# Kernel tuning notes

Hardware: AMD Instinct MI355X
Metric: run time of the kernel (lower is better)

The kernel has to match this reference:

```python
import jax, jax.numpy as jnp
import numpy as np
from jax import lax

N, D, H, E = 8192, 1024, 4096, 8


def setup_inputs() -> dict:
    key = jax.random.key(0)
    ks = jax.random.split(key, 4)
    return {
        "x": jax.random.normal(ks[0], (N, D), dtype=jnp.float32),
        "wg": jax.random.normal(ks[1], (D, E), dtype=jnp.float32) * 0.001,
        "fc1_w": jax.random.normal(ks[2], (E, D, H), dtype=jnp.float32) * 0.001,
        "fc1_b": jnp.zeros((E, 1, H), dtype=jnp.float32),
        "fc2_w": jax.random.normal(ks[3], (E, H, D), dtype=jnp.float32) * 0.001,
        "fc2_b": jnp.zeros((E, 1, D), dtype=jnp.float32),
        "k": 2,
    }


def reference(x, wg, fc1_w, fc1_b, fc2_w, fc2_b, k):
    n, d = x.shape
    e = wg.shape[1]
    cap = (k * n) // e  # expert capacity (capacity factor 1.0)

    # --- gate ---
    scores = jax.nn.softmax(x @ wg, axis=-1)          # [N,E]
    topv, topi = lax.top_k(scores, k)                 # [N,k]

    # --- top-k routing: position of each (token, slot) within its expert buffer ---
    masks = jax.nn.one_hot(topi, e, dtype=jnp.int32)  # [N,k,E]
    # slot-major priority: all slot-0 assignments before slot-1
    m = jnp.transpose(masks, (1, 0, 2)).reshape(k * n, e)
    pos_flat = jnp.cumsum(m, axis=0) - m              # position before own assignment
    pos = jnp.sum(pos_flat * m, axis=1).reshape(k, n).T   # [N,k]
    valid = pos < cap                                  # capacity overflow -> dropped

    # --- load-balance aux loss (top-1 fraction * mean gate prob) ---
    me = scores.mean(axis=0)                           # [E]
    ce = masks[:, 0, :].astype(scores.dtype).mean(axis=0)
    l_aux = e * jnp.sum(me * ce)

    # --- encode (dispatch): scatter tokens into [E, C, D] buffers ---
    w = valid.astype(x.dtype)                          # [N,k]
    flat_idx = topi * cap + jnp.where(valid, pos, 0)   # [N,k]
    contrib = (x[:, None, :] * w[:, :, None]).reshape(-1, d)
    dispatched = jnp.zeros((e * cap, d), x.dtype).at[flat_idx.reshape(-1)].add(contrib)
    dispatched = dispatched.reshape(e, cap, d)

    # --- batched expert FFN (all-to-all is identity on one device) ---
    h = jax.nn.relu(jnp.einsum('ecd,edh->ech', dispatched, fc1_w) + fc1_b)
    y = jnp.einsum('ech,ehd->ecd', h, fc2_w) + fc2_b   # [E,C,D]

    # --- decode (combine): gather back and weight by gate scores ---
    gathered = y.reshape(e * cap, d)[flat_idx]         # [N,k,D]
    output = jnp.einsum('nk,nkd->nd', topv * w, gathered)
    return output, l_aux
```

## Files before the change

kernel.cpp:

```cpp
#include <hip/hip_runtime.h>
#include <hip/hip_bf16.h>
#include <stdint.h>

#define N_TOK 8192
#define DMODEL 1024
#define HDIM 4096
#define NEXP 8
#define CAP 2048
#define GATE_BLOCKS (N_TOK / 4)

typedef float floatx4 __attribute__((ext_vector_type(4)));
typedef int int32x4_t __attribute__((ext_vector_type(4)));
typedef int int32x8_t __attribute__((ext_vector_type(8)));

static __device__ __forceinline__ void async_copy16(const void* g, void* l) {
  __builtin_amdgcn_global_load_lds(
      (const __attribute__((address_space(1))) void*)g,
      (__attribute__((address_space(3))) void*)l, 16, 0, 0);
}

static __device__ __forceinline__ unsigned int pk4_fp8(float a, float b, float c, float d) {
  int r = __builtin_amdgcn_cvt_pk_fp8_f32(a, b, 0, 0);
  r = __builtin_amdgcn_cvt_pk_fp8_f32(c, d, r, 1);
  return (unsigned int)r;
}

static __device__ __forceinline__ unsigned short f2bf(float f) {
  union { float f; uint32_t u; } v; v.f = f;
  uint32_t r = (v.u + 0x7FFFu + ((v.u >> 16) & 1u)) >> 16;
  return (unsigned short)r;
}

static __device__ __forceinline__ float bf2f(unsigned short u) {
  union { float f; uint32_t u32; } v; v.u32 = ((uint32_t)u) << 16;
  return v.f;
}

__global__ __launch_bounds__(256) void gate_kernel(
    const float* __restrict__ x, const float* __restrict__ wg,
    float* __restrict__ topv, int* __restrict__ topi,
    float* __restrict__ me_part, int* __restrict__ ce_part) {
  __shared__ float sm_p[4][NEXP];
  __shared__ int sm_i0[4];
  int wave = threadIdx.x >> 6;
  int lane = threadIdx.x & 63;
  int n = blockIdx.x * 4 + wave;
  float acc[NEXP];
#pragma unroll
  for (int e = 0; e < NEXP; e++) acc[e] = 0.f;
  const float* xr = x + (size_t)n * DMODEL;
#pragma unroll 4
  for (int i = 0; i < DMODEL / 64; i++) {
    int idx = lane + 64 * i;
    float xv = xr[idx];
    const float4* wr = (const float4*)(wg + (size_t)idx * NEXP);
    float4 w0 = wr[0], w1 = wr[1];
    acc[0] += xv * w0.x; acc[1] += xv * w0.y;
    acc[2] += xv * w0.z; acc[3] += xv * w0.w;
    acc[4] += xv * w1.x; acc[5] += xv * w1.y;
    acc[6] += xv * w1.z; acc[7] += xv * w1.w;
  }
#pragma unroll
  for (int e = 0; e < NEXP; e++) {
    float v = acc[e];
#pragma unroll
    for (int off = 32; off > 0; off >>= 1) v += __shfl_down(v, off, 64);
    acc[e] = v;
  }
  if (lane == 0) {
    float mx = acc[0];
#pragma unroll
    for (int e = 1; e < NEXP; e++) mx = fmaxf(mx, acc[e]);
    float p[NEXP]; float s = 0.f;
#pragma unroll
    for (int e = 0; e < NEXP; e++) { p[e] = expf(acc[e] - mx); s += p[e]; }
    float inv = 1.f / s;
#pragma unroll
    for (int e = 0; e < NEXP; e++) p[e] *= inv;
    int i0 = 0; float v0 = p[0];
#pragma unroll
    for (int e = 1; e < NEXP; e++) if (p[e] > v0) { v0 = p[e]; i0 = e; }
    int i1 = -1; float v1 = -1.f;
#pragma unroll
    for (int e = 0; e < NEXP; e++) {
      if (e == i0) continue;
      if (p[e] > v1) { v1 = p[e]; i1 = e; }
    }
    topv[n * 2] = v0; topv[n * 2 + 1] = v1;
    topi[n * 2] = i0; topi[n * 2 + 1] = i1;
#pragma unroll
    for (int e = 0; e < NEXP; e++) sm_p[wave][e] = p[e];
    sm_i0[wave] = i0;
  }
  __syncthreads();
  if (threadIdx.x < NEXP) {
    int e = threadIdx.x;
    float pm = 0.f; int cc = 0;
#pragma unroll
    for (int w = 0; w < 4; w++) {
      pm += sm_p[w][e];
      cc += (sm_i0[w] == e) ? 1 : 0;
    }
    me_part[blockIdx.x * NEXP + e] = pm;
    ce_part[blockIdx.x * NEXP + e] = cc;
  }
}

__global__ __launch_bounds__(1024) void scan_kernel(
    const int* __restrict__ topi, const float* __restrict__ topv,
    int* __restrict__ flat_idx, float* __restrict__ cw,
    const float* __restrict__ me_part, const int* __restrict__ ce_part,
    float* __restrict__ out_laux) {
  __shared__ int hist[16][NEXP];
  __shared__ int base[NEXP];
  __shared__ float redm[NEXP][2];
  __shared__ float redc[NEXP][2];
  int tid = threadIdx.x;
  int w = tid >> 6, lane = tid & 63;
  if (tid < NEXP) base[tid] = 0;
  int vals[16];
#pragma unroll
  for (int c = 0; c < 16; c++) {
    int j = c * 1024 + tid;
    vals[c] = topi[(size_t)(j & 8191) * 2 + (j >> 13)];
  }
  __syncthreads();
  for (int c = 0; c < 16; c++) {
    int j = c * 1024 + tid;
    int slot = j >> 13;
    int n = j & 8191;
    int e = vals[c];
    int rank = 0;
#pragma unroll
    for (int ee = 0; ee < NEXP; ee++) {
      unsigned long long m = __ballot(e == ee);
      if (e == ee) rank = __popcll(m & ((1ull << lane) - 1ull));
      if (lane == ee) hist[w][ee] = __popcll(m);
    }
    __syncthreads();
    if (tid < NEXP) {
      int run = base[tid];
#pragma unroll
      for (int ww = 0; ww < 16; ww++) {
        int t = hist[ww][tid];
        hist[ww][tid] = run;
        run += t;
      }
      base[tid] = run;
    }
    __syncthreads();
    int pos = hist[w][e] + rank;
    bool valid = pos < CAP;
    flat_idx[n * 2 + slot] = e * CAP + (valid ? pos : 0);
    cw[n * 2 + slot] = valid ? topv[n * 2 + slot] : 0.f;
    __syncthreads();
  }
  {
    int e2 = tid >> 7, c2 = tid & 127;
    float pm = 0.f, cc = 0.f;
    for (int b = c2; b < GATE_BLOCKS; b += 128) {
      pm += me_part[b * NEXP + e2];
      cc += (float)ce_part[b * NEXP + e2];
    }
#pragma unroll
    for (int off = 32; off > 0; off >>= 1) {
      pm += __shfl_down(pm, off, 64);
      cc += __shfl_down(cc, off, 64);
    }
    if ((tid & 63) == 0) {
      redm[e2][(tid >> 6) & 1] = pm;
      redc[e2][(tid >> 6) & 1] = cc;
    }
    __syncthreads();
    if (tid == 0) {
      float s = 0.f;
#pragma unroll
      for (int ee = 0; ee < NEXP; ee++) {
        float tm2 = redm[ee][0] + redm[ee][1];
        float tc2 = redc[ee][0] + redc[ee][1];
        s += (tm2 / (float)N_TOK) * (tc2 / (float)N_TOK);
      }
      *out_laux = (float)NEXP * s;
    }
  }
}

__global__ __launch_bounds__(256) void transpose_cvt_fp8_both(
    const float* __restrict__ in1, unsigned char* __restrict__ out1,
    const float* __restrict__ in2, unsigned char* __restrict__ out2) {
  __shared__ float tile[32][129];
  int z = blockIdx.z;
  const float* in; unsigned char* out; int R, C, bx, by, zz;
  if (z < 8) {
    in = in1; out = out1; R = DMODEL; C = HDIM; zz = z;
    bx = blockIdx.x; by = blockIdx.y;
  } else {
    in = in2; out = out2; R = HDIM; C = DMODEL; zz = z - 8;
    bx = blockIdx.x & 31; by = blockIdx.y * 4 + (blockIdx.x >> 5);
  }
  const float* inp = in + (size_t)zz * R * C;
  unsigned char* outp = out + (size_t)zz * R * C;
  int c0 = bx * 32, r0 = by * 128;
  int t = threadIdx.x;
#pragma unroll
  for (int p = 0; p < 4; p++) {
    int r = p * 32 + (t >> 3);
    int c4 = (t & 7) * 4;
    float4 v = *(const float4*)(inp + (size_t)(r0 + r) * C + c0 + c4);
    tile[c4 + 0][r] = v.x; tile[c4 + 1][r] = v.y;
    tile[c4 + 2][r] = v.z; tile[c4 + 3][r] = v.w;
  }
  __syncthreads();
  int c = t >> 3, r16 = (t & 7) * 16;
  unsigned int w[4];
#pragma unroll
  for (int j = 0; j < 4; j++) {
    float a = tile[c][r16 + j * 4 + 0] * 512.f;
    float b = tile[c][r16 + j * 4 + 1] * 512.f;
    float cc2 = tile[c][r16 + j * 4 + 2] * 512.f;
    float d = tile[c][r16 + j * 4 + 3] * 512.f;
    w[j] = pk4_fp8(a, b, cc2, d);
  }
  uint4 o; o.x = w[0]; o.y = w[1]; o.z = w[2]; o.w = w[3];
  *(uint4*)(outp + (size_t)(c0 + c) * R + r0 + r16) = o;
}

__global__ __launch_bounds__(64) void dispatch_kernel(
    const float* __restrict__ x, const int* __restrict__ flat_idx,
    const float* __restrict__ cw, unsigned char* __restrict__ disp) {
  int a = blockIdx.x;
  if (cw[a] == 0.f) return;
  int n = a >> 1;
  int f = flat_idx[a];
  int lane = threadIdx.x;
  const float4* xr = (const float4*)(x + (size_t)n * DMODEL);
  unsigned int* dr = (unsigned int*)(disp + (size_t)f * DMODEL);
#pragma unroll
  for (int i = 0; i < 4; i++) {
    float4 v = xr[lane + 64 * i];
    dr[lane + 64 * i] = pk4_fp8(v.x, v.y, v.z, v.w);
  }
}

template <int K_DIM, bool RELU, int OUT_MODE>
__global__ __launch_bounds__(256) void gemm_fp8_kernel(
    const unsigned char* __restrict__ A, const unsigned char* __restrict__ BT,
    const float* __restrict__ bias, void* __restrict__ Cout, int M, int Ncols,
    float inv_scale, float out_mult) {
  constexpr int BK = 128;
  constexpr int NSTAGE = K_DIM / BK;
  static_assert(NSTAGE >= 2, "need >=2 K stages for the 2-deep pipeline");
  __shared__ unsigned char As[2][128 * BK];
  __shared__ unsigned char Bs[2][128 * BK];

  int e = blockIdx.z, tm = blockIdx.y, tn = blockIdx.x;
  const unsigned char* Ae = A + (size_t)e * M * K_DIM + (size_t)tm * 128 * K_DIM;
  const unsigned char* Be = BT + (size_t)e * Ncols * K_DIM + (size_t)tn * 128 * K_DIM;
  int wv = threadIdx.x >> 6, l = threadIdx.x & 63;
  int wm = wv >> 1, wn = wv & 1;
  int l15 = l & 15, quad = l >> 4;
  int rbase = wv * 8 + (l >> 3);
  int cg = (l & 7) ^ ((l >> 3) & 7);
  floatx4 acc[4][4] = {};

#define STAGE_LOADS(k0, buf)                                                   \
  {                                                                            \
    _Pragma("unroll") for (int i = 0; i < 4; i++) {                            \
      int r = rbase + i * 32;                                                  \
      async_copy16(Ae + (size_t)r * K_DIM + (k0) + cg * 16,                    \
                   &As[buf][i * 4096 + wv * 1024]);                            \
      async_copy16(Be + (size_t)r * K_DIM + (k0) + cg * 16,                    \
                   &Bs[buf][i * 4096 + wv * 1024]);                            \
    }                                                                          \
  }

#define READ_AF(mi)                                                            \
  {                                                                            \
    int m = wm * 64 + (mi) * 16 + l15;                                         \
    int x0 = (quad * 2) ^ (m & 7), x1 = (quad * 2 + 1) ^ (m & 7);              \
    int32x4_t lo = *(const int32x4_t*)(&As[cur][m * 128 + x0 * 16]);           \
    int32x4_t hi = *(const int32x4_t*)(&As[cur][m * 128 + x1 * 16]);           \
    af[mi] = __builtin_shufflevector(lo, hi, 0, 1, 2, 3, 4, 5, 6, 7);          \
  }

  STAGE_LOADS(0, 0);
  STAGE_LOADS(BK, 1);
#pragma unroll
  for (int s = 0; s < NSTAGE; s++) {
    const int cur = s & 1;
    if (s + 1 < NSTAGE)
      asm volatile("s_waitcnt vmcnt(8)" ::: "memory");
    else
      asm volatile("s_waitcnt vmcnt(0)" ::: "memory");
    __builtin_amdgcn_s_barrier();
    int32x8_t af[4], bf[4];
#pragma unroll
    for (int ni = 0; ni < 4; ni++) {
      int m = wn * 64 + ni * 16 + l15;
      int x0 = (quad * 2) ^ (m & 7), x1 = (quad * 2 + 1) ^ (m & 7);
      int32x4_t lo = *(const int32x4_t*)(&Bs[cur][m * 128 + x0 * 16]);
      int32x4_t hi = *(const int32x4_t*)(&Bs[cur][m * 128 + x1 * 16]);
      bf[ni] = __builtin_shufflevector(lo, hi, 0, 1, 2, 3, 4, 5, 6, 7);
    }
    READ_AF(0);
    __builtin_amdgcn_sched_barrier(0);
    READ_AF(1);
    READ_AF(2);
    READ_AF(3);
    __builtin_amdgcn_sched_barrier(0);
    __builtin_amdgcn_s_setprio(1);
    asm volatile("s_waitcnt lgkmcnt(6)" ::: "memory");
    __builtin_amdgcn_sched_barrier(0);
#pragma unroll
    for (int ni = 0; ni < 4; ni++)
      acc[0][ni] = __builtin_amdgcn_mfma_scale_f32_16x16x128_f8f6f4(
          af[0], bf[ni], acc[0][ni], 0, 0, 0, 0x7F7F7F7F, 0, 0x7F7F7F7F);
    asm volatile("s_waitcnt lgkmcnt(4)" ::: "memory");
    __builtin_amdgcn_sched_barrier(0);
#pragma unroll
    for (int ni = 0; ni < 4; ni++)
      acc[1][ni] = __builtin_amdgcn_mfma_scale_f32_16x16x128_f8f6f4(
          af[1], bf[ni], acc[1][ni], 0, 0, 0, 0x7F7F7F7F, 0, 0x7F7F7F7F);
    asm volatile("s_waitcnt lgkmcnt(2)" ::: "memory");
    __builtin_amdgcn_sched_barrier(0);
#pragma unroll
    for (int ni = 0; ni < 4; ni++)
      acc[2][ni] = __builtin_amdgcn_mfma_scale_f32_16x16x128_f8f6f4(
          af[2], bf[ni], acc[2][ni], 0, 0, 0, 0x7F7F7F7F, 0, 0x7F7F7F7F);
    asm volatile("s_waitcnt lgkmcnt(0)" ::: "memory");
    __builtin_amdgcn_sched_barrier(0);
    __builtin_amdgcn_s_setprio(0);
    __builtin_amdgcn_s_barrier();
    if (s + 2 < NSTAGE) STAGE_LOADS((s + 2) * BK, cur);
    __builtin_amdgcn_s_setprio(1);
#pragma unroll
    for (int ni = 0; ni < 4; ni++)
      acc[3][ni] = __builtin_amdgcn_mfma_scale_f32_16x16x128_f8f6f4(
          af[3], bf[ni], acc[3][ni], 0, 0, 0, 0x7F7F7F7F, 0, 0x7F7F7F7F);
    __builtin_amdgcn_s_setprio(0);
  }
#undef STAGE_LOADS
#undef READ_AF

  int row_base = tm * 128 + wm * 64;
  int col_base = tn * 128 + wn * 64;
  const float* be = bias + (size_t)e * Ncols;
#pragma unroll
  for (int ni = 0; ni < 4; ni++) {
    int col = col_base + ni * 16 + l15;
    float bv = be[col];
#pragma unroll
    for (int mi = 0; mi < 4; mi++) {
#pragma unroll
      for (int r = 0; r < 4; r++) {
        int row = row_base + mi * 16 + quad * 4 + r;
        float v = acc[mi][ni][r] * inv_scale + bv;
        if (RELU) v = fmaxf(v, 0.f);
        size_t idx = (size_t)e * M * Ncols + (size_t)row * Ncols + col;
        if (OUT_MODE == 1) {
          float s = fminf(fmaxf(v * out_mult, -440.f), 440.f);
          unsigned int b8 = (unsigned int)__builtin_amdgcn_cvt_pk_fp8_f32(s, s, 0, 0) & 0xFF;
          ((unsigned char*)Cout)[idx] = (unsigned char)b8;
        } else if (OUT_MODE == 2) {
          ((unsigned short*)Cout)[idx] = f2bf(v);
        } else {
          ((float*)Cout)[idx] = v;
        }
      }
    }
  }
}

__global__ __launch_bounds__(256) void combine_kernel(
    const unsigned short* __restrict__ y, const int* __restrict__ flat_idx,
    const float* __restrict__ cw, float* __restrict__ out) {
  int n = blockIdx.x;
  float w0 = cw[n * 2], w1 = cw[n * 2 + 1];
  int f0 = flat_idx[n * 2], f1 = flat_idx[n * 2 + 1];
  const ushort2* y0 = (const ushort2*)(y + (size_t)f0 * DMODEL);
  const ushort2* y1 = (const ushort2*)(y + (size_t)f1 * DMODEL);
  float2* o = (float2*)(out + (size_t)n * DMODEL);
  int t = threadIdx.x;
#pragma unroll
  for (int i = 0; i < 2; i++) {
    int j = t + i * 256;
    ushort2 a = y0[j], b = y1[j];
    float2 r;
    r.x = w0 * bf2f(a.x) + w1 * bf2f(b.x);
    r.y = w0 * bf2f(a.y) + w1 * bf2f(b.y);
    o[j] = r;
  }
}

extern "C" void kernel_launch(void* const* d_in, const int* in_sizes, int n_in,
                              void* d_out, int out_size, void* d_ws,
                              size_t ws_size, hipStream_t stream) {
  (void)in_sizes; (void)n_in; (void)out_size; (void)ws_size;
  const float* x     = (const float*)d_in[0];
  const float* wg    = (const float*)d_in[1];
  const float* fc1_w = (const float*)d_in[2];
  const float* fc1_b = (const float*)d_in[3];
  const float* fc2_w = (const float*)d_in[4];
  const float* fc2_b = (const float*)d_in[5];
  float* out = (float*)d_out;

  char* ws = (char*)d_ws;
  size_t o = 0;
  unsigned char* fc1t = (unsigned char*)(ws + o); o += (size_t)NEXP * DMODEL * HDIM;
  unsigned char* fc2t = (unsigned char*)(ws + o); o += (size_t)NEXP * DMODEL * HDIM;
  unsigned char* disp = (unsigned char*)(ws + o); o += (size_t)NEXP * CAP * DMODEL;
  unsigned char* hbuf = (unsigned char*)(ws + o); o += (size_t)NEXP * CAP * HDIM;
  unsigned short* ybuf = (unsigned short*)(ws + o); o += (size_t)NEXP * CAP * DMODEL * 2;
  float* topv = (float*)(ws + o); o += (size_t)N_TOK * 2 * 4;
  int* topi   = (int*)(ws + o);   o += (size_t)N_TOK * 2 * 4;
  int* flat   = (int*)(ws + o);   o += (size_t)N_TOK * 2 * 4;
  float* cw   = (float*)(ws + o); o += (size_t)N_TOK * 2 * 4;
  float* mep  = (float*)(ws + o); o += (size_t)GATE_BLOCKS * NEXP * 4;
  int* cep    = (int*)(ws + o);   o += (size_t)GATE_BLOCKS * NEXP * 4;


  gate_kernel<<<GATE_BLOCKS, 256, 0, stream>>>(x, wg, topv, topi, mep, cep);
  scan_kernel<<<1, 1024, 0, stream>>>(topi, topv, flat, cw, mep, cep,
                                      out + (size_t)N_TOK * DMODEL);
  transpose_cvt_fp8_both<<<dim3(128, 8, 16), 256, 0, stream>>>(fc1_w, fc1t, fc2_w, fc2t);
  dispatch_kernel<<<N_TOK * 2, 64, 0, stream>>>(x, flat, cw, disp);
  gemm_fp8_kernel<DMODEL, true, 1>
      <<<dim3(HDIM / 128, CAP / 128, NEXP), 256, 0, stream>>>(
          disp, fc1t, fc1_b, hbuf, CAP, HDIM, 1.f / 512.f, 16.f);
  gemm_fp8_kernel<HDIM, false, 2>
      <<<dim3(DMODEL / 128, CAP / 128, NEXP), 256, 0, stream>>>(
          hbuf, fc2t, fc2_b, ybuf, CAP, DMODEL, 1.f / 8192.f, 1.f);
  combine_kernel<<<N_TOK, 256, 0, stream>>>(ybuf, flat, cw, out);
}
```

Before: 576.9 us.

## Fuse gate into weight transpose launch and remap GEMM blocks across XCDs

Merges the gate scoring kernel into the fc1/fc2 fp8 transpose-convert kernel as extra z-slices of one grid, removing a launch and letting the small gate work overlap with the bandwidth-heavy weight conversion. Separately, the fp8 GEMM now remaps linear block IDs so that consecutive logical tiles, which share operand rows, land on the same XCD (8-way round-robin), aiming to improve L2 reuse. The fused kernel carries the larger shared tile for all blocks, which could lower occupancy for the gate blocks. The scan kernel now runs after the transpose, where it previously ran before it.

Measured after the change: 550.4 us. 1.05x faster.

```diff
diff --git a/kernel.cpp b/kernel.cpp
--- a/kernel.cpp
+++ b/kernel.cpp
@@ -36,15 +36,56 @@
   return v.f;
 }
 
-__global__ __launch_bounds__(256) void gate_kernel(
+__global__ __launch_bounds__(256) void gate_transpose_kernel(
+    const float* __restrict__ fc1_w, unsigned char* __restrict__ fc1t,
+    const float* __restrict__ fc2_w, unsigned char* __restrict__ fc2t,
     const float* __restrict__ x, const float* __restrict__ wg,
     float* __restrict__ topv, int* __restrict__ topi,
     float* __restrict__ me_part, int* __restrict__ ce_part) {
+  __shared__ float tile[32][129];
   __shared__ float sm_p[4][NEXP];
   __shared__ int sm_i0[4];
+  int z = blockIdx.z;
+  if (z < 16) {
+    const float* in; unsigned char* out; int R, C, bx, by, zz;
+    if (z < 8) {
+      in = fc1_w; out = fc1t; R = DMODEL; C = HDIM; zz = z;
+      bx = blockIdx.x; by = blockIdx.y;
+    } else {
+      in = fc2_w; out = fc2t; R = HDIM; C = DMODEL; zz = z - 8;
+      bx = blockIdx.x & 31; by = blockIdx.y * 4 + (blockIdx.x >> 5);
+    }
+    const float* inp = in + (size_t)zz * R * C;
+    unsigned char* outp = out + (size_t)zz * R * C;
+    int c0 = bx * 32, r0 = by * 128;
+    int t = threadIdx.x;
+#pragma unroll
+    for (int p = 0; p < 4; p++) {
+      int r = p * 32 + (t >> 3);
+      int c4 = (t & 7) * 4;
+      float4 v = *(const float4*)(inp + (size_t)(r0 + r) * C + c0 + c4);
+      tile[c4 + 0][r] = v.x; tile[c4 + 1][r] = v.y;
+      tile[c4 + 2][r] = v.z; tile[c4 + 3][r] = v.w;
+    }
+    __syncthreads();
+    int c = t >> 3, r16 = (t & 7) * 16;
+    unsigned int w[4];
+#pragma unroll
+    for (int j = 0; j < 4; j++) {
+      float a = tile[c][r16 + j * 4 + 0] * 512.f;
+      float b = tile[c][r16 + j * 4 + 1] * 512.f;
+      float cc2 = tile[c][r16 + j * 4 + 2] * 512.f;
+      float d = tile[c][r16 + j * 4 + 3] * 512.f;
+      w[j] = pk4_fp8(a, b, cc2, d);
+    }
+    uint4 o; o.x = w[0]; o.y = w[1]; o.z = w[2]; o.w = w[3];
+    *(uint4*)(outp + (size_t)(c0 + c) * R + r0 + r16) = o;
+    return;
+  }
+  int gb = (z - 16) * 1024 + blockIdx.y * 128 + blockIdx.x;
   int wave = threadIdx.x >> 6;
   int lane = threadIdx.x & 63;
-  int n = blockIdx.x * 4 + wave;
+  int n = gb * 4 + wave;
   float acc[NEXP];
 #pragma unroll
   for (int e = 0; e < NEXP; e++) acc[e] = 0.f;
@@ -101,8 +142,8 @@
       pm += sm_p[w][e];
       cc += (sm_i0[w] == e) ? 1 : 0;
     }
-    me_part[blockIdx.x * NEXP + e] = pm;
-    ce_part[blockIdx.x * NEXP + e] = cc;
+    me_part[gb * NEXP + e] = pm;
+    ce_part[gb * NEXP + e] = cc;
   }
 }
 
@@ -185,46 +226,6 @@
   }
 }
 
-__global__ __launch_bounds__(256) void transpose_cvt_fp8_both(
-    const float* __restrict__ in1, unsigned char* __restrict__ out1,
-    const float* __restrict__ in2, unsigned char* __restrict__ out2) {
-  __shared__ float tile[32][129];
-  int z = blockIdx.z;
-  const float* in; unsigned char* out; int R, C, bx, by, zz;
-  if (z < 8) {
-    in = in1; out = out1; R = DMODEL; C = HDIM; zz = z;
-    bx = blockIdx.x; by = blockIdx.y;
-  } else {
-    in = in2; out = out2; R = HDIM; C = DMODEL; zz = z - 8;
-    bx = blockIdx.x & 31; by = blockIdx.y * 4 + (blockIdx.x >> 5);
-  }
-  const float* inp = in + (size_t)zz * R * C;
-  unsigned char* outp = out + (size_t)zz * R * C;
-  int c0 = bx * 32, r0 = by * 128;
-  int t = threadIdx.x;
-#pragma unroll
-  for (int p = 0; p < 4; p++) {
-    int r = p * 32 + (t >> 3);
-    int c4 = (t & 7) * 4;
-    float4 v = *(const float4*)(inp + (size_t)(r0 + r) * C + c0 + c4);
-    tile[c4 + 0][r] = v.x; tile[c4 + 1][r] = v.y;
-    tile[c4 + 2][r] = v.z; tile[c4 + 3][r] = v.w;
-  }
-  __syncthreads();
-  int c = t >> 3, r16 = (t & 7) * 16;
-  unsigned int w[4];
-#pragma unroll
-  for (int j = 0; j < 4; j++) {
-    float a = tile[c][r16 + j * 4 + 0] * 512.f;
-    float b = tile[c][r16 + j * 4 + 1] * 512.f;
-    float cc2 = tile[c][r16 + j * 4 + 2] * 512.f;
-    float d = tile[c][r16 + j * 4 + 3] * 512.f;
-    w[j] = pk4_fp8(a, b, cc2, d);
-  }
-  uint4 o; o.x = w[0]; o.y = w[1]; o.z = w[2]; o.w = w[3];
-  *(uint4*)(outp + (size_t)(c0 + c) * R + r0 + r16) = o;
-}
-
 __global__ __launch_bounds__(64) void dispatch_kernel(
     const float* __restrict__ x, const int* __restrict__ flat_idx,
     const float* __restrict__ cw, unsigned char* __restrict__ disp) {
@@ -253,7 +254,22 @@
   __shared__ unsigned char As[2][128 * BK];
   __shared__ unsigned char Bs[2][128 * BK];
 
-  int e = blockIdx.z, tm = blockIdx.y, tn = blockIdx.x;
+  unsigned gx = gridDim.x;
+  unsigned gxy = gridDim.x * gridDim.y;
+  unsigned nwg = gxy * gridDim.z;
+  unsigned lid = blockIdx.z * gxy + blockIdx.y * gx + blockIdx.x;
+  int e, tm, tn;
+  if ((nwg & 7u) == 0u) {
+    unsigned chunk = nwg >> 3;
+    unsigned w = (lid & 7u) * chunk + (lid >> 3);
+    e = w / gxy;
+    unsigned rem = w - (unsigned)e * gxy;
+    tm = rem / gx;
+    tn = rem - (unsigned)tm * gx;
+  } else {
+    e = blockIdx.z; tm = blockIdx.y; tn = blockIdx.x;
+  }
+
   const unsigned char* Ae = A + (size_t)e * M * K_DIM + (size_t)tm * 128 * K_DIM;
   const unsigned char* Be = BT + (size_t)e * Ncols * K_DIM + (size_t)tn * 128 * K_DIM;
   int wv = threadIdx.x >> 6, l = threadIdx.x & 63;
@@ -419,10 +435,10 @@
   int* cep    = (int*)(ws + o);   o += (size_t)GATE_BLOCKS * NEXP * 4;
 
 
-  gate_kernel<<<GATE_BLOCKS, 256, 0, stream>>>(x, wg, topv, topi, mep, cep);
+  gate_transpose_kernel<<<dim3(128, 8, 18), 256, 0, stream>>>(
+      fc1_w, fc1t, fc2_w, fc2t, x, wg, topv, topi, mep, cep);
   scan_kernel<<<1, 1024, 0, stream>>>(topi, topv, flat, cw, mep, cep,
                                       out + (size_t)N_TOK * DMODEL);
-  transpose_cvt_fp8_both<<<dim3(128, 8, 16), 256, 0, stream>>>(fc1_w, fc1t, fc2_w, fc2t);
   dispatch_kernel<<<N_TOK * 2, 64, 0, stream>>>(x, flat, cw, disp);
   gemm_fp8_kernel<DMODEL, true, 1>
       <<<dim3(HDIM / 128, CAP / 128, NEXP), 256, 0, stream>>>(
```
